# Kernel optimization log

Hardware: AMD Instinct MI355X
Metric: run time of the kernel (lower is better)

Reference implementation:

```python
import jax, jax.numpy as jnp
import numpy as np

PRIME = 2147483647  # 2^31 - 1, MinHash modulus
GAMMA = 0.3
NUM_HEADS = 8


def minhash_sketch(ids, a, b):
    # ids: (B, L, S) int64 atom ids; a,b: (K,) hash coefficients
    # h[b,l,s,k] = (a[k]*id + b[k]) mod PRIME ; signature = min over the set axis S
    h = (ids[..., None] * a + b) % PRIME          # (B, L, S, K)
    return h.min(axis=2)                          # (B, L, K)


def jaccard_from_signatures(sig_q, sig_k):
    # sig_q: (B, Lq, K), sig_k: (B, Lk, K) -> (B, Lq, Lk) fraction of matching slots.
    # Scan over the K hash slots to avoid materializing a (B,Lq,Lk,K) tensor.
    B, Lq, K = sig_q.shape
    Lk = sig_k.shape[1]

    def step(acc, cols):
        qc, kc = cols                              # (B,Lq), (B,Lk)
        return acc + (qc[:, :, None] == kc[:, None, :]).astype(jnp.float32), None

    init = jnp.zeros((B, Lq, Lk), jnp.float32)
    xs = (jnp.moveaxis(sig_q, -1, 0), jnp.moveaxis(sig_k, -1, 0))
    acc, _ = jax.lax.scan(step, init, xs)
    return acc / K


def symdiff_from_jaccard(jacc, size_q, size_k):
    # |A ∩ B| = J/(1+J) * (|A|+|B|)  =>  |A Δ B| = (|A|+|B|) * (1-J)/(1+J)
    tot = size_q[:, :, None] + size_k[:, None, :]   # (B, Lq, Lk)
    return tot * (1.0 - jacc) / (1.0 + jacc)


def setup_inputs() -> dict:
    key = jax.random.key(0)
    ks = jax.random.split(key, 12)
    B, Lq, Lk, E, S, K, V = 4, 1024, 1024, 512, 8, 128, 32000
    w = lambda k: (jax.random.normal(k, (E, E), jnp.float32) * 0.02)
    return {
        "query": jax.random.normal(ks[0], (B, Lq, E), jnp.float32),
        "key": jax.random.normal(ks[1], (B, Lk, E), jnp.float32),
        "value": jax.random.normal(ks[2], (B, Lk, E), jnp.float32),
        "token_sets_q": jax.random.randint(ks[3], (B, Lq, S), 0, V).astype(jnp.int64),
        "token_sets_k": jax.random.randint(ks[4], (B, Lk, S), 0, V).astype(jnp.int64),
        "hash_a": jax.random.randint(ks[5], (K,), 1, PRIME - 1).astype(jnp.int64),
        "hash_b": jax.random.randint(ks[6], (K,), 0, PRIME - 1).astype(jnp.int64),
        "Wq": w(ks[7]), "bq": jnp.zeros((E,), jnp.float32),
        "Wk": w(ks[8]), "bk": jnp.zeros((E,), jnp.float32),
        "Wv": w(ks[9]), "bv": jnp.zeros((E,), jnp.float32),
        "Wo": w(ks[10]), "bo": jnp.zeros((E,), jnp.float32),
    }


def reference(query, key, value, token_sets_q, token_sets_k, hash_a, hash_b,
              Wq, bq, Wk, bk, Wv, bv, Wo, bo):
    B, Lq, E = query.shape
    Lk = key.shape[1]
    H = NUM_HEADS
    d = E // H

    # in-projections (torch Linear: x @ W^T + b); q,k are computed but the
    # attention scores come solely from the token-set kernel (gating disabled)
    q = query @ Wq.T + bq
    k = key @ Wk.T + bk
    v = (value @ Wv.T + bv).reshape(B, Lk, H, d).transpose(0, 2, 1, 3)  # (B,H,Lk,d)

    # MinHash sketches of per-token atom sets -> estimated Jaccard -> Δ-RBF score
    sig_q = minhash_sketch(token_sets_q, hash_a, hash_b)   # (B,Lq,K)
    sig_k = minhash_sketch(token_sets_k, hash_a, hash_b)   # (B,Lk,K)
    jacc = jaccard_from_signatures(sig_q, sig_k)           # (B,Lq,Lk)

    S = token_sets_q.shape[-1]
    size_q = jnp.full((B, Lq), S, jnp.float32)             # uniform CSR offsets -> |set| = S
    size_k = jnp.full((B, Lk), S, jnp.float32)
    delta = symdiff_from_jaccard(jacc, size_q, size_k)
    scores = jnp.exp(-GAMMA * delta)                       # (B,Lq,Lk), shared by all heads

    attn = jax.nn.softmax(scores, axis=-1)                 # no masks, no causal, dropout=0
    ctx = jnp.einsum('bqk,bhkd->bqhd', attn, v).reshape(B, Lq, E)
    return ctx @ Wo.T + bo
```

## Files before the change

kernel.cpp:

```cpp
#include <hip/hip_runtime.h>
#include <hip/hip_bf16.h>
#include <stdint.h>

#define PRIME 2147483647u
#define GAMMA 0.3f
#define K_HASH 128
#define S_SET 8
#define NB 4
#define LQ 1024
#define LK 1024
#define EDIM 512
#define FIX_CAP (NB * LQ * LK)

typedef unsigned short ushort_t;
typedef __attribute__((ext_vector_type(8))) short short8;
typedef __attribute__((ext_vector_type(4))) float f32x4;

static __device__ __forceinline__ unsigned short f2bf(float f) {
    unsigned u = __builtin_bit_cast(unsigned, f);
    u += 0x7FFFu + ((u >> 16) & 1u);
    return (unsigned short)(u >> 16);
}

static __device__ __forceinline__ void glds16(const void* g, void* l) {
    __builtin_amdgcn_global_load_lds(
        (const __attribute__((address_space(1))) unsigned int*)g,
        (__attribute__((address_space(3))) unsigned int*)l, 16, 0, 0);
}

#define SWZ(r) ((((r) >> 2) & 3) ^ ((r) & 3))

static __device__ __forceinline__ float score_of(int m) {
    float r = (float)(K_HASH - m) / (float)(K_HASH + m);
    return expf(expf(-GAMMA * (2.0f * S_SET) * r));
}

#define EPI_ROWBIAS  0
#define EPI_COLBIAS  2
#define EPI_NONE     3
#define EPI_DIVBIAS  4

template<int OUTF32, int MODE>
static __device__ void gemm64_dev(
        const ushort_t* __restrict__ A, const ushort_t* __restrict__ B,
        void* __restrict__ C,
        const float* __restrict__ bias, const float* __restrict__ scale,
        int lda, int ldb, int ldc, int Kd, int m0, int n0,
        ushort_t* AsBase, ushort_t* BsBase, int tid) {
    ushort_t (*As)[64 * 32] = (ushort_t (*)[64 * 32])AsBase;
    ushort_t (*Bs)[64 * 32] = (ushort_t (*)[64 * 32])BsBase;
    int w = tid >> 6, lane = tid & 63;
    int wm = (w & 1) * 32, wn = (w >> 1) * 32;
    int mrow = lane & 15, kg = lane >> 4;

    int r = tid >> 2, c = (tid & 3) ^ SWZ(r);
    const ushort_t* pa = A + (size_t)(m0 + r) * lda + c * 8;
    const ushort_t* pb = B + (size_t)(n0 + r) * ldb + c * 8;

    int aoff[2], boff[2];
    #pragma unroll
    for (int s = 0; s < 2; s++) {
        int Ra = wm + s * 16 + mrow;
        aoff[s] = Ra * 32 + (kg ^ SWZ(Ra)) * 8;
        int Rb = wn + s * 16 + mrow;
        boff[s] = Rb * 32 + (kg ^ SWZ(Rb)) * 8;
    }

    f32x4 acc[2][2] = {};
    int nK = Kd >> 5;
    glds16(pa, &As[0][tid * 8]);
    glds16(pb, &Bs[0][tid * 8]);
    for (int i = 0; i < nK; i++) {
        __syncthreads();
        int cur = i & 1, nxt = cur ^ 1;
        if (i + 1 < nK) {
            int k0 = (i + 1) << 5;
            glds16(pa + k0, &As[nxt][tid * 8]);
            glds16(pb + k0, &Bs[nxt][tid * 8]);
        }
        short8 af[2], bh[2];
        #pragma unroll
        for (int s = 0; s < 2; s++) {
            af[s] = *(const short8*)&As[cur][aoff[s]];
            bh[s] = *(const short8*)&Bs[cur][boff[s]];
        }
        #pragma unroll
        for (int ii = 0; ii < 2; ii++)
            #pragma unroll
            for (int jj = 0; jj < 2; jj++)
                acc[ii][jj] = __builtin_amdgcn_mfma_f32_16x16x32_bf16(
                                  af[ii], bh[jj], acc[ii][jj], 0, 0, 0);
    }

    int col = lane & 15, rbase = (lane >> 4) * 4;
    #pragma unroll
    for (int ii = 0; ii < 2; ii++) {
        #pragma unroll
        for (int jj = 0; jj < 2; jj++) {
            #pragma unroll
            for (int rr = 0; rr < 4; rr++) {
                int gm = m0 + wm + ii * 16 + rbase + rr;
                int gn = n0 + wn + jj * 16 + col;
                float v = acc[ii][jj][rr];
                if (MODE == EPI_ROWBIAS)      v += bias[gm];
                else if (MODE == EPI_COLBIAS) v += bias[gn];
                else if (MODE == EPI_DIVBIAS) v = v / scale[gm] + bias[gn];
                size_t cix = (size_t)gm * ldc + gn;
                if (OUTF32) ((float*)C)[cix] = v;
                else        ((ushort_t*)C)[cix] = f2bf(v);
            }
        }
    }
}

#define CVT_N0 (NB * LK * EDIM)
#define CVT_N1 (EDIM * EDIM)
#define CVT_N2 (EDIM * EDIM)
#define CVT_BLOCKS ((CVT_N0 + CVT_N1 + CVT_N2) / (256 * 8))
#define PF_BLOCKS 2048
#define MZ_BLOCKS 1024
#define RS_BLOCKS 16
#define SIGT_BLOCKS 128
#define PREP_GRID (CVT_BLOCKS + PF_BLOCKS + MZ_BLOCKS + RS_BLOCKS + SIGT_BLOCKS)

__global__ __launch_bounds__(256) void prep_kernel(
        const float* __restrict__ v, const float* __restrict__ wv,
        const float* __restrict__ wo,
        ushort_t* __restrict__ vb, ushort_t* __restrict__ wvb,
        ushort_t* __restrict__ wob,
        const int* __restrict__ ts_q, const int* __restrict__ ts_k,
        const int* __restrict__ ha, const int* __restrict__ hb,
        unsigned* __restrict__ sigTq, unsigned* __restrict__ sigTk,
        uint8_t* __restrict__ M, ushort_t* __restrict__ P,
        float* __restrict__ rs, unsigned* __restrict__ nfix) {
    __shared__ unsigned tile[128 * 65];
    __shared__ int ids_s[64 * S_SET];
    int blk = blockIdx.x, tid = threadIdx.x;
    if (blk < CVT_BLOCKS) {
        size_t i = ((size_t)blk * 256 + tid) * 8;
        const float* src; ushort_t* dst; size_t off;
        if (i < CVT_N0)                { src = v;  dst = vb;  off = i; }
        else if (i < CVT_N0 + CVT_N1)  { src = wv; dst = wvb; off = i - CVT_N0; }
        else                           { src = wo; dst = wob; off = i - CVT_N0 - CVT_N1; }
        float4 a = *(const float4*)(src + off);
        float4 b = *(const float4*)(src + off + 4);
        ushort4 o0, o1;
        o0.x = f2bf(a.x); o0.y = f2bf(a.y); o0.z = f2bf(a.z); o0.w = f2bf(a.w);
        o1.x = f2bf(b.x); o1.y = f2bf(b.y); o1.z = f2bf(b.z); o1.w = f2bf(b.w);
        *(ushort4*)(dst + off)     = o0;
        *(ushort4*)(dst + off + 4) = o1;
        return;
    }
    if (blk < CVT_BLOCKS + PF_BLOCKS) {
        unsigned short pb = f2bf(score_of(0));
        unsigned wpat = (unsigned)pb | ((unsigned)pb << 16);
        size_t off = ((size_t)(blk - CVT_BLOCKS) * 256 + tid) * 16;
        *(int4*)((char*)P + off) = (int4){(int)wpat, (int)wpat, (int)wpat, (int)wpat};
        return;
    }
    if (blk < CVT_BLOCKS + PF_BLOCKS + MZ_BLOCKS) {
        size_t off = ((size_t)(blk - CVT_BLOCKS - PF_BLOCKS) * 256 + tid) * 16;
        *(int4*)(M + off) = (int4){0, 0, 0, 0};
        return;
    }
    if (blk < CVT_BLOCKS + PF_BLOCKS + MZ_BLOCKS + RS_BLOCKS) {
        int i = (blk - CVT_BLOCKS - PF_BLOCKS - MZ_BLOCKS) * 256 + tid;
        rs[i] = (float)LK * score_of(0);
        if (i == 0) *nfix = 0u;
        return;
    }
    int sb = blk - (CVT_BLOCKS + PF_BLOCKS + MZ_BLOCKS + RS_BLOCKS);
    int r0 = sb * 64;
    const int* ts = (r0 < NB * LQ) ? ts_q : ts_k;
    unsigned* sigT = (r0 < NB * LQ) ? sigTq : sigTk;
    int base = r0 & (NB * LQ - 1);
    ((int2*)ids_s)[tid] = ((const int2*)(ts + (size_t)base * S_SET))[tid];
    __syncthreads();
    int kt = tid & 127, rt = tid >> 7;
    unsigned long long a  = (unsigned)ha[kt];
    unsigned long long bb = (unsigned)hb[kt];
    for (int r = rt; r < 64; r += 2) {
        unsigned mn = 0xFFFFFFFFu;
        #pragma unroll
        for (int s = 0; s < S_SET; s++) {
            unsigned long long x =
                a * (unsigned long long)(unsigned)ids_s[r * S_SET + s] + bb;
            x = (x & PRIME) + (x >> 31);
            x = (x & PRIME) + (x >> 31);
            unsigned rr = (unsigned)x;
            if (rr >= PRIME) rr -= PRIME;
            mn = (rr < mn) ? rr : mn;
        }
        tile[kt * 65 + r] = mn;
    }
    __syncthreads();
    #pragma unroll
    for (int ch = 0; ch < 32; ch++) {
        int idx = ch * 256 + tid;
        int k = idx >> 6, r = idx & 63;
        sigT[(size_t)k * (NB * LQ) + base + r] = tile[k * 65 + r];
    }
}

union JSmem {
    struct { unsigned keys[2048]; ushort_t vals[2048]; } j;
    struct { ushort_t As[2][64 * 32]; ushort_t Bs[2][64 * 32]; } g;
};

__global__ __launch_bounds__(256) void joing1_kernel(
        const unsigned* __restrict__ sigTq, const unsigned* __restrict__ sigTk,
        uint8_t* __restrict__ M, unsigned* __restrict__ fixlist,
        unsigned* __restrict__ nfix,
        const ushort_t* __restrict__ Wvb, const ushort_t* __restrict__ Vb,
        ushort_t* __restrict__ Vproj, const float* __restrict__ bv) {
    __shared__ JSmem sm;
    int blk = blockIdx.x, tid = threadIdx.x;
    int grp = blk >> 8;
    int t = (grp >> 1) * 256 + (blk & 255);
    if (grp & 1) {
        gemm64_dev<0, EPI_COLBIAS>(Vb, Wvb, Vproj, bv, nullptr,
                                   EDIM, EDIM, EDIM, EDIM,
                                   (t >> 3) * 64, (t & 7) * 64,
                                   sm.g.As[0], sm.g.Bs[0], tid);
        return;
    }
    int b = t >> 7, k = t & 127;
    const unsigned* kc = sigTk + (size_t)k * (NB * LK) + b * LK;
    const unsigned* qc = sigTq + (size_t)k * (NB * LQ) + b * LQ;
    uint4 kv = ((const uint4*)kc)[tid];
    uint4 qv = ((const uint4*)qc)[tid];
    #pragma unroll
    for (int i = 0; i < 8; i++) sm.j.keys[i * 256 + tid] = 0xFFFFFFFFu;
    __syncthreads();
    unsigned kvv[4] = {kv.x, kv.y, kv.z, kv.w};
    #pragma unroll
    for (int e = 0; e < 4; e++) {
        unsigned vv = kvv[e];
        unsigned h = (vv * 2654435761u) >> 21;
        while (true) {
            unsigned prev = atomicCAS(&sm.j.keys[h], 0xFFFFFFFFu, vv);
            if (prev == 0xFFFFFFFFu) { sm.j.vals[h] = (ushort_t)(tid * 4 + e); break; }
            h = (h + 1) & 2047;
        }
    }
    __syncthreads();
    uint8_t* Mb = M + ((size_t)b << 20);
    unsigned qvv[4] = {qv.x, qv.y, qv.z, qv.w};
    #pragma unroll
    for (int e = 0; e < 4; e++) {
        unsigned vv = qvv[e];
        unsigned h = (vv * 2654435761u) >> 21, kk;
        while ((kk = sm.j.keys[h]) != 0xFFFFFFFFu) {
            if (kk == vv) {
                unsigned ix = ((unsigned)(tid * 4 + e) << 10) + sm.j.vals[h];
                unsigned sh = (ix & 3u) * 8;
                unsigned old = atomicAdd((unsigned*)(Mb + (ix & ~3u)), 1u << sh);
                if (((old >> sh) & 0xFFu) == 0u) {
                    unsigned slot = atomicAdd(nfix, 1u);
                    if (slot < (unsigned)FIX_CAP)
                        fixlist[slot] = ((unsigned)b << 20) | ix;
                }
            }
            h = (h + 1) & 2047;
        }
    }
}

__global__ __launch_bounds__(256) void g1bfix_kernel(
        const ushort_t* __restrict__ Wob, const ushort_t* __restrict__ Vproj,
        ushort_t* __restrict__ W2t,
        const uint8_t* __restrict__ M, const unsigned* __restrict__ fixlist,
        const unsigned* __restrict__ nfix,
        ushort_t* __restrict__ P, float* __restrict__ rs) {
    __shared__ ushort_t As[2][64 * 32], Bs[2][64 * 32];
    int blk = blockIdx.x, tid = threadIdx.x;
    if (blk < 512) {
        gemm64_dev<0, EPI_NONE>(Wob, Vproj, W2t, nullptr, nullptr,
                                EDIM, EDIM, NB * LK, EDIM,
                                (blk >> 6) * 64, (blk & 63) * 64,
                                As[0], Bs[0], tid);
        return;
    }
    unsigned n = *nfix;
    if (n > (unsigned)FIX_CAP) n = FIX_CAP;
    float p0 = score_of(0);
    for (unsigned i = (unsigned)(blk - 512) * 256 + tid; i < n; i += 64 * 256) {
        unsigned e = fixlist[i];
        int b = e >> 20;
        unsigned ix = e & 0xFFFFFu;
        int m = M[((size_t)b << 20) + ix];
        float p = score_of(m);
        P[((size_t)b << 20) + ix] = f2bf(p);
        atomicAdd(&rs[(b << 10) + (ix >> 10)], p - p0);
    }
}

template<int OUTF32, int MODE>
__global__ __launch_bounds__(256) void btgemm_kernel(
        const ushort_t* __restrict__ A, const ushort_t* __restrict__ B,
        void* __restrict__ C,
        const float* __restrict__ bias, const float* __restrict__ scale,
        int lda, int ldb, int ldc, int Kd,
        long long sA, long long sB, long long sC, long long sS) {
    __shared__ ushort_t As[2][64 * 32], Bs[2][64 * 32];
    int z = blockIdx.z;
    gemm64_dev<OUTF32, MODE>(
        A + (size_t)z * sA, B + (size_t)z * sB,
        (char*)C + (size_t)z * sC * (OUTF32 ? 4 : 2),
        bias, scale + (size_t)z * sS,
        lda, ldb, ldc, Kd, blockIdx.y * 64, blockIdx.x * 64,
        As[0], Bs[0], threadIdx.x);
}

extern "C" void kernel_launch(void* const* d_in, const int* in_sizes, int n_in,
                              void* d_out, int out_size, void* d_ws, size_t ws_size,
                              hipStream_t stream) {
    const float* value = (const float*)d_in[2];
    const int* tsq = (const int*)d_in[3];
    const int* tsk = (const int*)d_in[4];
    const int* ha  = (const int*)d_in[5];
    const int* hb  = (const int*)d_in[6];
    const float* Wv = (const float*)d_in[11];
    const float* bv = (const float*)d_in[12];
    const float* Wo = (const float*)d_in[13];
    const float* bo = (const float*)d_in[14];
    float* out = (float*)d_out;

    char* ws = (char*)d_ws;
    unsigned* sigTq = (unsigned*)(ws);
    unsigned* sigTk = (unsigned*)(ws + (2ull << 20));
    uint8_t*  M     = (uint8_t*)(ws + (4ull << 20));
    ushort_t* P     = (ushort_t*)(ws + (8ull << 20));
    float*    rs    = (float*)(ws + (16ull << 20));
    unsigned* nfix  = (unsigned*)(ws + (16ull << 20) + (32ull << 10));
    unsigned* fixl  = (unsigned*)(ws + (17ull << 20));
    ushort_t* Vproj = (ushort_t*)(ws + (33ull << 20));
    ushort_t* W2t   = (ushort_t*)(ws + (37ull << 20));
    ushort_t* Vb    = (ushort_t*)(ws + (41ull << 20));
    ushort_t* Wvb   = (ushort_t*)(ws + (45ull << 20));
    ushort_t* Wob   = (ushort_t*)(ws + (45ull << 20) + (512ull << 10));

    prep_kernel<<<PREP_GRID, 256, 0, stream>>>(
        value, Wv, Wo, Vb, Wvb, Wob, tsq, tsk, ha, hb, sigTq, sigTk,
        M, P, rs, nfix);

    joing1_kernel<<<1024, 256, 0, stream>>>(
        sigTq, sigTk, M, fixl, nfix, Wvb, Vb, Vproj, bv);

    g1bfix_kernel<<<576, 256, 0, stream>>>(
        Wob, Vproj, W2t, M, fixl, nfix, P, rs);

    btgemm_kernel<1, EPI_DIVBIAS><<<dim3(EDIM / 64, LQ / 64, NB), 256, 0, stream>>>(
        P, W2t, out, bo, rs,
        LK, NB * LK, EDIM, LK,
        (long long)LQ * LK, (long long)LK, (long long)LQ * EDIM, (long long)LQ);
}
```

Baseline: 183.3 us.

## Replace dense P·W2 GEMM with sparse match-list accumulation over a precombined Wv·Wo

Drops the dense bf16 score matrix P and the batched P×W2 GEMM. The output is rewritten as p0 times the column sum of V·Wv^T·Wo^T, plus a sparse correction taken only over (q,k) pairs that have nonzero match counts, using a precomputed W2c = Vb·(Wo·Wv)^T. It also folds bv into an output bias, precomputes the row sums of V, and removes the fix-list and atomic row-sum passes. The per-row sparse gather in outk is serial per block and depends on match sparsity. It also changes where bf16 rounding happens relative to the reference.

Result: faster. 177.6 us (-3.1%).

```diff
diff --git a/kernel.cpp b/kernel.cpp
--- a/kernel.cpp
+++ b/kernel.cpp
@@ -10,7 +10,6 @@
 #define LQ 1024
 #define LK 1024
 #define EDIM 512
-#define FIX_CAP (NB * LQ * LK)
 
 typedef unsigned short ushort_t;
 typedef __attribute__((ext_vector_type(8))) short short8;
@@ -35,16 +34,12 @@
     return expf(expf(-GAMMA * (2.0f * S_SET) * r));
 }
 
-#define EPI_ROWBIAS  0
-#define EPI_COLBIAS  2
-#define EPI_NONE     3
-#define EPI_DIVBIAS  4
+#define EPI_NONE 3
 
 template<int OUTF32, int MODE>
 static __device__ void gemm64_dev(
         const ushort_t* __restrict__ A, const ushort_t* __restrict__ B,
         void* __restrict__ C,
-        const float* __restrict__ bias, const float* __restrict__ scale,
         int lda, int ldb, int ldc, int Kd, int m0, int n0,
         ushort_t* AsBase, ushort_t* BsBase, int tid) {
     ushort_t (*As)[64 * 32] = (ushort_t (*)[64 * 32])AsBase;
@@ -102,9 +97,6 @@
                 int gm = m0 + wm + ii * 16 + rbase + rr;
                 int gn = n0 + wn + jj * 16 + col;
                 float v = acc[ii][jj][rr];
-                if (MODE == EPI_ROWBIAS)      v += bias[gm];
-                else if (MODE == EPI_COLBIAS) v += bias[gn];
-                else if (MODE == EPI_DIVBIAS) v = v / scale[gm] + bias[gn];
                 size_t cix = (size_t)gm * ldc + gn;
                 if (OUTF32) ((float*)C)[cix] = v;
                 else        ((ushort_t*)C)[cix] = f2bf(v);
@@ -115,33 +107,34 @@
 
 #define CVT_N0 (NB * LK * EDIM)
 #define CVT_N1 (EDIM * EDIM)
-#define CVT_N2 (EDIM * EDIM)
-#define CVT_BLOCKS ((CVT_N0 + CVT_N1 + CVT_N2) / (256 * 8))
-#define PF_BLOCKS 2048
+#define CVT_BLOCKS ((CVT_N0 + CVT_N1) / (256 * 8))
 #define MZ_BLOCKS 1024
-#define RS_BLOCKS 16
 #define SIGT_BLOCKS 128
-#define PREP_GRID (CVT_BLOCKS + PF_BLOCKS + MZ_BLOCKS + RS_BLOCKS + SIGT_BLOCKS)
+#define VBS_BLOCKS 16
+#define WVT_BLOCKS 64
+#define BOB_BLOCKS 2
+#define PREP_GRID (CVT_BLOCKS + MZ_BLOCKS + SIGT_BLOCKS + VBS_BLOCKS + WVT_BLOCKS + BOB_BLOCKS)
 
 __global__ __launch_bounds__(256) void prep_kernel(
-        const float* __restrict__ v, const float* __restrict__ wv,
-        const float* __restrict__ wo,
-        ushort_t* __restrict__ vb, ushort_t* __restrict__ wvb,
-        ushort_t* __restrict__ wob,
+        const float* __restrict__ value, const float* __restrict__ Wv,
+        const float* __restrict__ Wo, const float* __restrict__ bv,
+        const float* __restrict__ bo,
+        ushort_t* __restrict__ Vb, ushort_t* __restrict__ Wob,
+        ushort_t* __restrict__ WvT,
         const int* __restrict__ ts_q, const int* __restrict__ ts_k,
         const int* __restrict__ ha, const int* __restrict__ hb,
         unsigned* __restrict__ sigTq, unsigned* __restrict__ sigTk,
-        uint8_t* __restrict__ M, ushort_t* __restrict__ P,
-        float* __restrict__ rs, unsigned* __restrict__ nfix) {
+        uint8_t* __restrict__ M, float* __restrict__ vbsum,
+        float* __restrict__ bob) {
     __shared__ unsigned tile[128 * 65];
     __shared__ int ids_s[64 * S_SET];
+    __shared__ float vs[256];
     int blk = blockIdx.x, tid = threadIdx.x;
     if (blk < CVT_BLOCKS) {
         size_t i = ((size_t)blk * 256 + tid) * 8;
         const float* src; ushort_t* dst; size_t off;
-        if (i < CVT_N0)                { src = v;  dst = vb;  off = i; }
-        else if (i < CVT_N0 + CVT_N1)  { src = wv; dst = wvb; off = i - CVT_N0; }
-        else                           { src = wo; dst = wob; off = i - CVT_N0 - CVT_N1; }
+        if (i < CVT_N0) { src = value; dst = Vb;  off = i; }
+        else            { src = Wo;    dst = Wob; off = i - CVT_N0; }
         float4 a = *(const float4*)(src + off);
         float4 b = *(const float4*)(src + off + 4);
         ushort4 o0, o1;
@@ -151,55 +144,80 @@
         *(ushort4*)(dst + off + 4) = o1;
         return;
     }
-    if (blk < CVT_BLOCKS + PF_BLOCKS) {
-        unsigned short pb = f2bf(score_of(0));
-        unsigned wpat = (unsigned)pb | ((unsigned)pb << 16);
+    if (blk < CVT_BLOCKS + MZ_BLOCKS) {
         size_t off = ((size_t)(blk - CVT_BLOCKS) * 256 + tid) * 16;
-        *(int4*)((char*)P + off) = (int4){(int)wpat, (int)wpat, (int)wpat, (int)wpat};
-        return;
-    }
-    if (blk < CVT_BLOCKS + PF_BLOCKS + MZ_BLOCKS) {
-        size_t off = ((size_t)(blk - CVT_BLOCKS - PF_BLOCKS) * 256 + tid) * 16;
         *(int4*)(M + off) = (int4){0, 0, 0, 0};
         return;
     }
-    if (blk < CVT_BLOCKS + PF_BLOCKS + MZ_BLOCKS + RS_BLOCKS) {
-        int i = (blk - CVT_BLOCKS - PF_BLOCKS - MZ_BLOCKS) * 256 + tid;
-        rs[i] = (float)LK * score_of(0);
-        if (i == 0) *nfix = 0u;
-        return;
-    }
-    int sb = blk - (CVT_BLOCKS + PF_BLOCKS + MZ_BLOCKS + RS_BLOCKS);
-    int r0 = sb * 64;
-    const int* ts = (r0 < NB * LQ) ? ts_q : ts_k;
-    unsigned* sigT = (r0 < NB * LQ) ? sigTq : sigTk;
-    int base = r0 & (NB * LQ - 1);
-    ((int2*)ids_s)[tid] = ((const int2*)(ts + (size_t)base * S_SET))[tid];
-    __syncthreads();
-    int kt = tid & 127, rt = tid >> 7;
-    unsigned long long a  = (unsigned)ha[kt];
-    unsigned long long bb = (unsigned)hb[kt];
-    for (int r = rt; r < 64; r += 2) {
-        unsigned mn = 0xFFFFFFFFu;
-        #pragma unroll
-        for (int s = 0; s < S_SET; s++) {
-            unsigned long long x =
-                a * (unsigned long long)(unsigned)ids_s[r * S_SET + s] + bb;
-            x = (x & PRIME) + (x >> 31);
-            x = (x & PRIME) + (x >> 31);
-            unsigned rr = (unsigned)x;
-            if (rr >= PRIME) rr -= PRIME;
-            mn = (rr < mn) ? rr : mn;
-        }
-        tile[kt * 65 + r] = mn;
-    }
-    __syncthreads();
-    #pragma unroll
-    for (int ch = 0; ch < 32; ch++) {
-        int idx = ch * 256 + tid;
-        int k = idx >> 6, r = idx & 63;
-        sigT[(size_t)k * (NB * LQ) + base + r] = tile[k * 65 + r];
-    }
+    if (blk < CVT_BLOCKS + MZ_BLOCKS + SIGT_BLOCKS) {
+        int sb = blk - (CVT_BLOCKS + MZ_BLOCKS);
+        int r0 = sb * 64;
+        const int* ts = (r0 < NB * LQ) ? ts_q : ts_k;
+        unsigned* sigT = (r0 < NB * LQ) ? sigTq : sigTk;
+        int base = r0 & (NB * LQ - 1);
+        ((int2*)ids_s)[tid] = ((const int2*)(ts + (size_t)base * S_SET))[tid];
+        __syncthreads();
+        int kt = tid & 127, rt = tid >> 7;
+        unsigned long long a  = (unsigned)ha[kt];
+        unsigned long long bb = (unsigned)hb[kt];
+        for (int r = rt; r < 64; r += 2) {
+            unsigned mn = 0xFFFFFFFFu;
+            #pragma unroll
+            for (int s = 0; s < S_SET; s++) {
+                unsigned long long x =
+                    a * (unsigned long long)(unsigned)ids_s[r * S_SET + s] + bb;
+                x = (x & PRIME) + (x >> 31);
+                x = (x & PRIME) + (x >> 31);
+                unsigned rr = (unsigned)x;
+                if (rr >= PRIME) rr -= PRIME;
+                mn = (rr < mn) ? rr : mn;
+            }
+            tile[kt * 65 + r] = mn;
+        }
+        __syncthreads();
+        #pragma unroll
+        for (int ch = 0; ch < 32; ch++) {
+            int idx = ch * 256 + tid;
+            int k = idx >> 6, r = idx & 63;
+            sigT[(size_t)k * (NB * LQ) + base + r] = tile[k * 65 + r];
+        }
+        return;
+    }
+    if (blk < CVT_BLOCKS + MZ_BLOCKS + SIGT_BLOCKS + VBS_BLOCKS) {
+        int vb = blk - (CVT_BLOCKS + MZ_BLOCKS + SIGT_BLOCKS);
+        int b = vb >> 2, ch = vb & 3;
+        int e = ch * 128 + (tid & 127), half = tid >> 7;
+        const float* vp = value + ((size_t)(b * LK) + half * 512) * EDIM + e;
+        float s = 0.f;
+        for (int j = 0; j < 512; j++) s += vp[(size_t)j * EDIM];
+        vs[tid] = s;
+        __syncthreads();
+        if (tid < 128) vbsum[b * EDIM + ch * 128 + tid] = vs[tid] + vs[tid + 128];
+        return;
+    }
+    if (blk < CVT_BLOCKS + MZ_BLOCKS + SIGT_BLOCKS + VBS_BLOCKS + WVT_BLOCKS) {
+        int wt = blk - (CVT_BLOCKS + MZ_BLOCKS + SIGT_BLOCKS + VBS_BLOCKS);
+        int r0 = (wt >> 3) * 64, c0 = (wt & 7) * 64;
+        ushort_t (*tt)[65] = (ushort_t (*)[65])tile;
+        #pragma unroll
+        for (int p = 0; p < 16; p++) {
+            int idx = p * 256 + tid, r = idx >> 6, c = idx & 63;
+            tt[c][r] = f2bf(Wv[(size_t)(r0 + r) * EDIM + c0 + c]);
+        }
+        __syncthreads();
+        #pragma unroll
+        for (int p = 0; p < 16; p++) {
+            int idx = p * 256 + tid, r = idx >> 6, c = idx & 63;
+            WvT[(size_t)(c0 + r) * EDIM + r0 + c] = tt[r][c];
+        }
+        return;
+    }
+    int bb = blk - (CVT_BLOCKS + MZ_BLOCKS + SIGT_BLOCKS + VBS_BLOCKS + WVT_BLOCKS);
+    int n = bb * 256 + tid;
+    const float* worow = Wo + (size_t)n * EDIM;
+    float acc = bo[n];
+    for (int e = 0; e < EDIM; e++) acc += bv[e] * worow[e];
+    bob[n] = acc;
 }
 
 union JSmem {
@@ -209,22 +227,32 @@
 
 __global__ __launch_bounds__(256) void joing1_kernel(
         const unsigned* __restrict__ sigTq, const unsigned* __restrict__ sigTk,
-        uint8_t* __restrict__ M, unsigned* __restrict__ fixlist,
-        unsigned* __restrict__ nfix,
-        const ushort_t* __restrict__ Wvb, const ushort_t* __restrict__ Vb,
-        ushort_t* __restrict__ Vproj, const float* __restrict__ bv) {
+        uint8_t* __restrict__ M,
+        const ushort_t* __restrict__ Wob, const ushort_t* __restrict__ WvT,
+        ushort_t* __restrict__ Wvo,
+        const float* __restrict__ vbsum, const float* __restrict__ Wv,
+        float* __restrict__ vpsum) {
     __shared__ JSmem sm;
     int blk = blockIdx.x, tid = threadIdx.x;
-    int grp = blk >> 8;
-    int t = (grp >> 1) * 256 + (blk & 255);
-    if (grp & 1) {
-        gemm64_dev<0, EPI_COLBIAS>(Vb, Wvb, Vproj, bv, nullptr,
-                                   EDIM, EDIM, EDIM, EDIM,
-                                   (t >> 3) * 64, (t & 7) * 64,
-                                   sm.g.As[0], sm.g.Bs[0], tid);
-        return;
-    }
-    int b = t >> 7, k = t & 127;
+    if (blk >= 512 + 64) {
+        int vb = blk - 576, b = vb >> 1;
+        int ep = (vb & 1) * 256 + tid;
+        const float* wvrow = Wv + (size_t)ep * EDIM;
+        const float* vbs = vbsum + b * EDIM;
+        float acc = 0.f;
+        for (int e = 0; e < EDIM; e++) acc += vbs[e] * wvrow[e];
+        vpsum[b * EDIM + ep] = acc;
+        return;
+    }
+    if (blk >= 512) {
+        int t = blk - 512;
+        gemm64_dev<0, EPI_NONE>(Wob, WvT, Wvo,
+                                EDIM, EDIM, EDIM, EDIM,
+                                (t >> 3) * 64, (t & 7) * 64,
+                                sm.g.As[0], sm.g.Bs[0], tid);
+        return;
+    }
+    int b = blk >> 7, k = blk & 127;
     const unsigned* kc = sigTk + (size_t)k * (NB * LK) + b * LK;
     const unsigned* qc = sigTq + (size_t)k * (NB * LQ) + b * LQ;
     uint4 kv = ((const uint4*)kc)[tid];
@@ -232,84 +260,111 @@
     #pragma unroll
     for (int i = 0; i < 8; i++) sm.j.keys[i * 256 + tid] = 0xFFFFFFFFu;
     __syncthreads();
-    unsigned kvv[4] = {kv.x, kv.y, kv.z, kv.w};
+    unsigned vvv[4] = {kv.x, kv.y, kv.z, kv.w};
+    unsigned hh[4]; bool dn[4];
     #pragma unroll
-    for (int e = 0; e < 4; e++) {
-        unsigned vv = kvv[e];
-        unsigned h = (vv * 2654435761u) >> 21;
-        while (true) {
-            unsigned prev = atomicCAS(&sm.j.keys[h], 0xFFFFFFFFu, vv);
-            if (prev == 0xFFFFFFFFu) { sm.j.vals[h] = (ushort_t)(tid * 4 + e); break; }
-            h = (h + 1) & 2047;
+    for (int e = 0; e < 4; e++) { hh[e] = (vvv[e] * 2654435761u) >> 21; dn[e] = false; }
+    int rem = 4;
+    while (rem) {
+        #pragma unroll
+        for (int e = 0; e < 4; e++) {
+            if (dn[e]) continue;
+            unsigned prev = atomicCAS(&sm.j.keys[hh[e]], 0xFFFFFFFFu, vvv[e]);
+            if (prev == 0xFFFFFFFFu) {
+                sm.j.vals[hh[e]] = (ushort_t)(tid * 4 + e);
+                dn[e] = true; rem--;
+            } else hh[e] = (hh[e] + 1) & 2047;
         }
     }
     __syncthreads();
     uint8_t* Mb = M + ((size_t)b << 20);
-    unsigned qvv[4] = {qv.x, qv.y, qv.z, qv.w};
+    unsigned qq[4] = {qv.x, qv.y, qv.z, qv.w};
     #pragma unroll
-    for (int e = 0; e < 4; e++) {
-        unsigned vv = qvv[e];
-        unsigned h = (vv * 2654435761u) >> 21, kk;
-        while ((kk = sm.j.keys[h]) != 0xFFFFFFFFu) {
-            if (kk == vv) {
-                unsigned ix = ((unsigned)(tid * 4 + e) << 10) + sm.j.vals[h];
-                unsigned sh = (ix & 3u) * 8;
-                unsigned old = atomicAdd((unsigned*)(Mb + (ix & ~3u)), 1u << sh);
-                if (((old >> sh) & 0xFFu) == 0u) {
-                    unsigned slot = atomicAdd(nfix, 1u);
-                    if (slot < (unsigned)FIX_CAP)
-                        fixlist[slot] = ((unsigned)b << 20) | ix;
+    for (int e = 0; e < 4; e++) { hh[e] = (qq[e] * 2654435761u) >> 21; dn[e] = false; }
+    rem = 4;
+    while (rem) {
+        unsigned kk[4];
+        #pragma unroll
+        for (int e = 0; e < 4; e++) kk[e] = sm.j.keys[hh[e]];
+        #pragma unroll
+        for (int e = 0; e < 4; e++) {
+            if (dn[e]) continue;
+            if (kk[e] == 0xFFFFFFFFu) { dn[e] = true; rem--; }
+            else {
+                if (kk[e] == qq[e]) {
+                    unsigned ix = ((unsigned)(tid * 4 + e) << 10) + sm.j.vals[hh[e]];
+                    atomicAdd((unsigned*)(Mb + (ix & ~3u)), 1u << ((ix & 3u) * 8));
                 }
+                hh[e] = (hh[e] + 1) & 2047;
             }
-            h = (h + 1) & 2047;
-        }
-    }
-}
-
-__global__ __launch_bounds__(256) void g1bfix_kernel(
-        const ushort_t* __restrict__ Wob, const ushort_t* __restrict__ Vproj,
-        ushort_t* __restrict__ W2t,
-        const uint8_t* __restrict__ M, const unsigned* __restrict__ fixlist,
-        const unsigned* __restrict__ nfix,
-        ushort_t* __restrict__ P, float* __restrict__ rs) {
+        }
+    }
+}
+
+__global__ __launch_bounds__(256) void g2_kernel(
+        const ushort_t* __restrict__ Vb, const ushort_t* __restrict__ Wvo,
+        ushort_t* __restrict__ W2c,
+        const float* __restrict__ vpsum, const float* __restrict__ Wo,
+        float* __restrict__ S) {
     __shared__ ushort_t As[2][64 * 32], Bs[2][64 * 32];
     int blk = blockIdx.x, tid = threadIdx.x;
-    if (blk < 512) {
-        gemm64_dev<0, EPI_NONE>(Wob, Vproj, W2t, nullptr, nullptr,
-                                EDIM, EDIM, NB * LK, EDIM,
-                                (blk >> 6) * 64, (blk & 63) * 64,
-                                As[0], Bs[0], tid);
-        return;
-    }
-    unsigned n = *nfix;
-    if (n > (unsigned)FIX_CAP) n = FIX_CAP;
+    if (blk >= 512) {
+        int sb = blk - 512, b = sb >> 1;
+        int n = (sb & 1) * 256 + tid;
+        const float* worow = Wo + (size_t)n * EDIM;
+        const float* vps = vpsum + b * EDIM;
+        float acc = 0.f;
+        for (int e = 0; e < EDIM; e++) acc += vps[e] * worow[e];
+        S[b * EDIM + n] = acc;
+        return;
+    }
+    gemm64_dev<0, EPI_NONE>(Vb, Wvo, W2c,
+                            EDIM, EDIM, EDIM, EDIM,
+                            (blk >> 3) * 64, (blk & 7) * 64,
+                            As[0], Bs[0], tid);
+}
+
+__global__ __launch_bounds__(256) void outk_kernel(
+        const uint8_t* __restrict__ M, const ushort_t* __restrict__ W2c,
+        const float* __restrict__ S, const float* __restrict__ bob,
+        float* __restrict__ out) {
+    __shared__ unsigned lj[256];
+    __shared__ float lp[256];
+    __shared__ unsigned lcnt;
+    int row = blockIdx.x, tid = threadIdx.x, b = row >> 10;
+    const uint8_t* Mr = M + ((size_t)row << 10);
     float p0 = score_of(0);
-    for (unsigned i = (unsigned)(blk - 512) * 256 + tid; i < n; i += 64 * 256) {
-        unsigned e = fixlist[i];
-        int b = e >> 20;
-        unsigned ix = e & 0xFFFFFu;
-        int m = M[((size_t)b << 20) + ix];
-        float p = score_of(m);
-        P[((size_t)b << 20) + ix] = f2bf(p);
-        atomicAdd(&rs[(b << 10) + (ix >> 10)], p - p0);
-    }
-}
-
-template<int OUTF32, int MODE>
-__global__ __launch_bounds__(256) void btgemm_kernel(
-        const ushort_t* __restrict__ A, const ushort_t* __restrict__ B,
-        void* __restrict__ C,
-        const float* __restrict__ bias, const float* __restrict__ scale,
-        int lda, int ldb, int ldc, int Kd,
-        long long sA, long long sB, long long sC, long long sS) {
-    __shared__ ushort_t As[2][64 * 32], Bs[2][64 * 32];
-    int z = blockIdx.z;
-    gemm64_dev<OUTF32, MODE>(
-        A + (size_t)z * sA, B + (size_t)z * sB,
-        (char*)C + (size_t)z * sC * (OUTF32 ? 4 : 2),
-        bias, scale + (size_t)z * sS,
-        lda, ldb, ldc, Kd, blockIdx.y * 64, blockIdx.x * 64,
-        As[0], Bs[0], threadIdx.x);
+    float acc0 = 0.f, acc1 = 0.f, drs = 0.f;
+    int n0 = tid * 2;
+    for (int c = 0; c < 4; c++) {
+        if (tid == 0) lcnt = 0;
+        __syncthreads();
+        uint8_t m = Mr[c * 256 + tid];
+        if (m) {
+            unsigned s = atomicAdd(&lcnt, 1u);
+            lj[s] = c * 256 + tid;
+            lp[s] = score_of((int)m) - p0;
+        }
+        __syncthreads();
+        unsigned cnt = lcnt;
+        for (unsigned i = 0; i < cnt; i++) {
+            float w = lp[i];
+            drs += w;
+            const ushort_t* wr = W2c + (((size_t)(b << 10) + lj[i]) << 9);
+            unsigned pk = *(const unsigned*)(wr + n0);
+            acc0 += w * __builtin_bit_cast(float, pk << 16);
+            acc1 += w * __builtin_bit_cast(float, pk & 0xFFFF0000u);
+        }
+        __syncthreads();
+    }
+    float rs = 1024.0f * p0 + drs;
+    float inv = 1.0f / rs;
+    float2 sv = *(const float2*)(S + b * EDIM + n0);
+    float2 bb = *(const float2*)(bob + n0);
+    float2 o;
+    o.x = (p0 * sv.x + acc0) * inv + bb.x;
+    o.y = (p0 * sv.y + acc1) * inv + bb.y;
+    *(float2*)(out + (size_t)row * EDIM + n0) = o;
 }
 
 extern "C" void kernel_launch(void* const* d_in, const int* in_sizes, int n_in,
@@ -330,28 +385,24 @@
     unsigned* sigTq = (unsigned*)(ws);
     unsigned* sigTk = (unsigned*)(ws + (2ull << 20));
     uint8_t*  M     = (uint8_t*)(ws + (4ull << 20));
-    ushort_t* P     = (ushort_t*)(ws + (8ull << 20));
-    float*    rs    = (float*)(ws + (16ull << 20));
-    unsigned* nfix  = (unsigned*)(ws + (16ull << 20) + (32ull << 10));
-    unsigned* fixl  = (unsigned*)(ws + (17ull << 20));
-    ushort_t* Vproj = (ushort_t*)(ws + (33ull << 20));
-    ushort_t* W2t   = (ushort_t*)(ws + (37ull << 20));
-    ushort_t* Vb    = (ushort_t*)(ws + (41ull << 20));
-    ushort_t* Wvb   = (ushort_t*)(ws + (45ull << 20));
-    ushort_t* Wob   = (ushort_t*)(ws + (45ull << 20) + (512ull << 10));
+    ushort_t* Vb    = (ushort_t*)(ws + (8ull << 20));
+    ushort_t* W2c   = (ushort_t*)(ws + (12ull << 20));
+    ushort_t* Wob   = (ushort_t*)(ws + (16ull << 20));
+    ushort_t* WvT   = (ushort_t*)(ws + (16ull << 20) + (512ull << 10));
+    ushort_t* Wvo   = (ushort_t*)(ws + (17ull << 20));
+    float* vbsum    = (float*)(ws + (17ull << 20) + (512ull << 10));
+    float* vpsum    = (float*)(ws + (17ull << 20) + (520ull << 10));
+    float* S        = (float*)(ws + (17ull << 20) + (528ull << 10));
+    float* bob      = (float*)(ws + (17ull << 20) + (536ull << 10));
 
     prep_kernel<<<PREP_GRID, 256, 0, stream>>>(
-        value, Wv, Wo, Vb, Wvb, Wob, tsq, tsk, ha, hb, sigTq, sigTk,
-        M, P, rs, nfix);
-
-    joing1_kernel<<<1024, 256, 0, stream>>>(
-        sigTq, sigTk, M, fixl, nfix, Wvb, Vb, Vproj, bv);
-
-    g1bfix_kernel<<<576, 256, 0, stream>>>(
-        Wob, Vproj, W2t, M, fixl, nfix, P, rs);
-
-    btgemm_kernel<1, EPI_DIVBIAS><<<dim3(EDIM / 64, LQ / 64, NB), 256, 0, stream>>>(
-        P, W2t, out, bo, rs,
-        LK, NB * LK, EDIM, LK,
-        (long long)LQ * LK, (long long)LK, (long long)LQ * EDIM, (long long)LQ);
-}
+        value, Wv, Wo, bv, bo, Vb, Wob, WvT,
+        tsq, tsk, ha, hb, sigTq, sigTk, M, vbsum, bob);
+
+    joing1_kernel<<<584, 256, 0, stream>>>(
+        sigTq, sigTk, M, Wob, WvT, Wvo, vbsum, Wv, vpsum);
+
+    g2_kernel<<<520, 256, 0, stream>>>(Vb, Wvo, W2c, vpsum, Wo, S);
+
+    outk_kernel<<<NB * LQ, 256, 0, stream>>>(M, W2c, S, bob, out);
+}
```
